# Performance work log

Hardware: AMD Instinct MI355X
Metric: run time of the kernel (lower is better)

The kernel has to match this reference:

```python
import jax, jax.numpy as jnp
import numpy as np

# Gemma config constants (layer_idx=0 -> 'sliding_attention')
H = 8          # num query heads
KVH = 4        # num kv heads
DH = 256       # head_dim
SW = 1024      # sliding_window
ROPE_BASE = 10000.0   # rope_local_base_freq (sliding layer)
EPS = 1e-6
SCALE = 256.0 ** -0.5  # query_pre_attn_scalar ** -0.5


def _rms_norm(x, w):
    # Gemma RMSNorm: fp32 norm, scale by (1 + w)
    x32 = x.astype(jnp.float32)
    n = x32 * jax.lax.rsqrt(jnp.mean(x32 * x32, axis=-1, keepdims=True) + EPS)
    return (n * (1.0 + w.astype(jnp.float32))).astype(x.dtype)


def _rope_cos_sin(S):
    inv_freq = 1.0 / (ROPE_BASE ** (jnp.arange(0, DH, 2, dtype=jnp.float32) / DH))
    freqs = jnp.outer(jnp.arange(S, dtype=jnp.float32), inv_freq)  # [S, DH/2]
    emb = jnp.concatenate([freqs, freqs], axis=-1)                 # [S, DH]
    return jnp.cos(emb), jnp.sin(emb)


def _rotate_half(x):
    x1, x2 = jnp.split(x, 2, axis=-1)
    return jnp.concatenate([-x2, x1], axis=-1)


def _apply_rope(x, cos, sin):
    # x: [B, H, S, DH]; cos/sin: [S, DH]
    return x * cos[None, None] + _rotate_half(x) * sin[None, None]


def setup_inputs() -> dict:
    key = jax.random.key(0)
    ks = jax.random.split(key, 7)
    B, S, D = 2, 2048, 2048
    w = lambda k, shape: jax.random.normal(k, shape, jnp.float32) * 0.02
    return {
        "hidden_states": jax.random.normal(ks[0], (B, S, D), jnp.float32),
        "Wq": w(ks[1], (H * DH, D)),
        "Wk": w(ks[2], (KVH * DH, D)),
        "Wv": w(ks[3], (KVH * DH, D)),
        "Wo": w(ks[4], (D, H * DH)),
        "q_norm_w": jnp.zeros((DH,), jnp.float32),
        "k_norm_w": jnp.zeros((DH,), jnp.float32),
    }


def reference(hidden_states, Wq, Wk, Wv, Wo, q_norm_w, k_norm_w):
    B, S, D = hidden_states.shape
    # projections (no bias)
    q = jnp.einsum("bsd,ed->bse", hidden_states, Wq).reshape(B, S, H, DH).transpose(0, 2, 1, 3)
    k = jnp.einsum("bsd,ed->bse", hidden_states, Wk).reshape(B, S, KVH, DH).transpose(0, 2, 1, 3)
    v = jnp.einsum("bsd,ed->bse", hidden_states, Wv).reshape(B, S, KVH, DH).transpose(0, 2, 1, 3)
    # Gemma q/k RMSNorm over head_dim, then RoPE (local base for sliding layer)
    q = _rms_norm(q, q_norm_w)
    k = _rms_norm(k, k_norm_w)
    cos, sin = _rope_cos_sin(S)
    q = _apply_rope(q, cos, sin)
    k = _apply_rope(k, cos, sin)
    # GQA: repeat kv heads
    rep = H // KVH
    k = jnp.repeat(k, rep, axis=1)
    v = jnp.repeat(v, rep, axis=1)
    # causal sliding-window mask
    i = jnp.arange(S)[:, None]
    j = jnp.arange(S)[None, :]
    mask = (j <= i) & (i - j < SW)  # [S, S]
    scores = jnp.einsum("bhqd,bhkd->bhqk", q, k) * SCALE
    scores = jnp.where(mask[None, None], scores, jnp.finfo(jnp.float32).min)
    attn = jax.nn.softmax(scores.astype(jnp.float32), axis=-1).astype(q.dtype)
    out = jnp.einsum("bhqk,bhkd->bhqd", attn, v)  # [B, H, S, DH]
    out = out.transpose(0, 2, 1, 3).reshape(B, S, H * DH)
    return jnp.einsum("bse,de->bsd", out, Wo)
```

## Files before the change

### kernel.cpp

```cpp
#include <hip/hip_runtime.h>
#include <hip/hip_bf16.h>


typedef __bf16 bf16x8 __attribute__((ext_vector_type(8)));
typedef __bf16 bf16x4 __attribute__((ext_vector_type(4)));
typedef float f32x4 __attribute__((ext_vector_type(4)));

#define NB 2
#define SEQ 2048
#define DMODEL 2048
#define NH 8
#define NKV 4
#define DHEAD 256
#define SWIN 1024

#define AS1 __attribute__((address_space(1)))
#define AS3 __attribute__((address_space(3)))

static __device__ __forceinline__ void gload_lds16(const void* g, void* l) {
    __builtin_amdgcn_global_load_lds((const AS1 void*)g, (AS3 void*)l, 16, 0, 0);
}

static __device__ __forceinline__ bf16x4 tr16(const __bf16* p) {
    bf16x4 r;
    asm volatile("ds_read_b64_tr_b16 %0, %1" : "=v"(r) : "v"((const AS3 __bf16*)p));
    return r;
}

__global__ void cvt_rope(const float* __restrict__ s0, const float* __restrict__ s1,
                         const float* __restrict__ s2, const float* __restrict__ s3,
                         const float* __restrict__ s4, __bf16* __restrict__ d0,
                         __bf16* __restrict__ d1, __bf16* __restrict__ d2,
                         __bf16* __restrict__ d3, __bf16* __restrict__ d4,
                         float* __restrict__ cosT, float* __restrict__ sinT) {
    if (blockIdx.x >= 20480) {
        int idx = (blockIdx.x - 20480) * 256 + threadIdx.x;
        int s = idx >> 7, i = idx & 127;
        float fr = (float)s * __expf(-(float)i * 0.0719557843f);
        cosT[idx] = cosf(fr);
        sinT[idx] = sinf(fr);
        return;
    }
    int i = blockIdx.x * 256 + threadIdx.x;
    const float* src; __bf16* dst;
    if (i < 2097152) { src = s0; dst = d0; }
    else if (i < 3145728) { i -= 2097152; src = s1; dst = d1; }
    else if (i < 3670016) { i -= 3145728; src = s2; dst = d2; }
    else if (i < 4194304) { i -= 3670016; src = s3; dst = d3; }
    else                  { i -= 4194304; src = s4; dst = d4; }
    f32x4 v = ((const f32x4*)src)[i];
    bf16x4 o;
#pragma unroll
    for (int j = 0; j < 4; ++j) o[j] = (__bf16)v[j];
    ((bf16x4*)dst)[i] = o;
}

template <int OUTBF16>
__global__ __launch_bounds__(512, 2)
void gemm_bt8(const __bf16* __restrict__ A, const __bf16* __restrict__ B,
              void* __restrict__ Cv, int M, int N, int K, int nbx) {
    __shared__ __align__(16) __bf16 sA[2][256 * 64];
    __shared__ __align__(16) __bf16 sB[2][256 * 64];
    const int tid = threadIdx.x;
    const int wave = tid >> 6, lane = tid & 63;
    const int lo = lane & 15, hi = lane >> 4;
    const int wm = wave >> 2, wn = wave & 3;
    const int qq = (int)gridDim.x >> 3;
    const int swz = ((int)blockIdx.x & 7) * qq + ((int)blockIdx.x >> 3);
    const int bx = swz % nbx, by = swz / nbx;
    const int brow = by * 256, bcol = bx * 256;
    const int xr = lo & 7;

    int aoff[4];
#pragma unroll
    for (int i = 0; i < 4; ++i) {
        int n = i * 512 + tid, r = n >> 3, s = n & 7;
        aoff[i] = r * K + ((s ^ (r & 7)) << 3);
    }
    const __bf16* Ab = A + (size_t)brow * K;
    const __bf16* Bb = B + (size_t)bcol * K;

    auto stgA = [&](int bsel, int kt, int h) {
        const __bf16* ga = Ab + kt * 64;
#pragma unroll
        for (int ii = 0; ii < 2; ++ii) {
            int i = h + ii * 2;
            gload_lds16(ga + aoff[i], (char*)&sA[bsel][0] + (i * 512 + wave * 64) * 16);
        }
    };
    auto stgB = [&](int bsel, int kt, int h) {
        const __bf16* gb = Bb + kt * 64;
#pragma unroll
        for (int i = 2 * h; i < 2 * h + 2; ++i)
            gload_lds16(gb + aoff[i], (char*)&sB[bsel][0] + (i * 512 + wave * 64) * 16);
    };

    f32x4 acc[8][4] = {};
    const int nt = K >> 6;

    stgA(0, 0, 0); stgA(0, 0, 1); stgB(0, 0, 0); stgB(0, 0, 1);
    stgA(1, 1, 0); stgA(1, 1, 1); stgB(1, 1, 0); stgB(1, 1, 1);
    asm volatile("s_waitcnt vmcnt(8)" ::: "memory");
    __builtin_amdgcn_s_barrier();

    for (int t = 0; t < nt; ++t) {
        const int buf = t & 1;
        const bool pre = (t + 2 < nt);
        const __bf16* sa = &sA[buf][0];
        const __bf16* sb = &sB[buf][0];
        bf16x8 af[8], b0[4], b1[4];
#pragma unroll
        for (int m = 0; m < 4; ++m)
#pragma unroll
            for (int ks = 0; ks < 2; ++ks)
                af[m * 2 + ks] = *(const bf16x8*)&sa[(wm * 128 + m * 16 + lo) * 64 + (((ks * 4 + hi) ^ xr) << 3)];
#pragma unroll
        for (int n = 0; n < 2; ++n)
#pragma unroll
            for (int ks = 0; ks < 2; ++ks)
                b0[n * 2 + ks] = *(const bf16x8*)&sb[(wn * 64 + n * 16 + lo) * 64 + (((ks * 4 + hi) ^ xr) << 3)];
        __builtin_amdgcn_sched_barrier(0);
        __builtin_amdgcn_s_barrier();
        __builtin_amdgcn_s_setprio(1);
#pragma unroll
        for (int m = 0; m < 4; ++m)
#pragma unroll
            for (int n = 0; n < 2; ++n)
#pragma unroll
                for (int ks = 0; ks < 2; ++ks)
                    acc[m][n] = __builtin_amdgcn_mfma_f32_16x16x32_bf16(af[m * 2 + ks], b0[n * 2 + ks], acc[m][n], 0, 0, 0);
        __builtin_amdgcn_s_setprio(0);
        __builtin_amdgcn_sched_barrier(0);
        __builtin_amdgcn_s_barrier();
#pragma unroll
        for (int n = 0; n < 2; ++n)
#pragma unroll
            for (int ks = 0; ks < 2; ++ks)
                b1[n * 2 + ks] = *(const bf16x8*)&sb[(wn * 64 + (n + 2) * 16 + lo) * 64 + (((ks * 4 + hi) ^ xr) << 3)];
        if (pre) stgA(buf, t + 2, 0);
        __builtin_amdgcn_sched_barrier(0);
        __builtin_amdgcn_s_barrier();
        __builtin_amdgcn_s_setprio(1);
#pragma unroll
        for (int m = 0; m < 4; ++m)
#pragma unroll
            for (int n = 0; n < 2; ++n)
#pragma unroll
                for (int ks = 0; ks < 2; ++ks)
                    acc[m][n + 2] = __builtin_amdgcn_mfma_f32_16x16x32_bf16(af[m * 2 + ks], b1[n * 2 + ks], acc[m][n + 2], 0, 0, 0);
        __builtin_amdgcn_s_setprio(0);
        __builtin_amdgcn_sched_barrier(0);
        __builtin_amdgcn_s_barrier();
#pragma unroll
        for (int m = 0; m < 4; ++m)
#pragma unroll
            for (int ks = 0; ks < 2; ++ks)
                af[m * 2 + ks] = *(const bf16x8*)&sa[(wm * 128 + (m + 4) * 16 + lo) * 64 + (((ks * 4 + hi) ^ xr) << 3)];
        if (pre) stgB(buf, t + 2, 1);
        __builtin_amdgcn_sched_barrier(0);
        __builtin_amdgcn_s_barrier();
        __builtin_amdgcn_s_setprio(1);
#pragma unroll
        for (int m = 0; m < 4; ++m)
#pragma unroll
            for (int n = 0; n < 2; ++n)
#pragma unroll
                for (int ks = 0; ks < 2; ++ks)
                    acc[m + 4][n + 2] = __builtin_amdgcn_mfma_f32_16x16x32_bf16(af[m * 2 + ks], b1[n * 2 + ks], acc[m + 4][n + 2], 0, 0, 0);
        __builtin_amdgcn_s_setprio(0);
        __builtin_amdgcn_sched_barrier(0);
        __builtin_amdgcn_s_barrier();
        if (pre) { stgA(buf, t + 2, 1); stgB(buf, t + 2, 0); }
        __builtin_amdgcn_sched_barrier(0);
        __builtin_amdgcn_s_setprio(1);
#pragma unroll
        for (int m = 0; m < 4; ++m)
#pragma unroll
            for (int n = 0; n < 2; ++n)
#pragma unroll
                for (int ks = 0; ks < 2; ++ks)
                    acc[m + 4][n] = __builtin_amdgcn_mfma_f32_16x16x32_bf16(af[m * 2 + ks], b0[n * 2 + ks], acc[m + 4][n], 0, 0, 0);
        __builtin_amdgcn_s_setprio(0);
        if (pre) asm volatile("s_waitcnt vmcnt(8)" ::: "memory");
        else     asm volatile("s_waitcnt vmcnt(0)" ::: "memory");
        __builtin_amdgcn_sched_barrier(0);
        __builtin_amdgcn_s_barrier();
    }

#pragma unroll
    for (int m = 0; m < 8; ++m) {
        int row = brow + wm * 128 + m * 16 + hi * 4;
#pragma unroll
        for (int n = 0; n < 4; ++n) {
            int col = bcol + wn * 64 + n * 16 + lo;
            if constexpr (OUTBF16) {
                __bf16* cp = (__bf16*)Cv + (size_t)row * N + col;
#pragma unroll
                for (int j = 0; j < 4; ++j)
                    cp[(size_t)j * N] = (__bf16)acc[m][n][j];
            } else {
                float* cp = (float*)Cv + (size_t)row * N + col;
#pragma unroll
                for (int j = 0; j < 4; ++j)
                    cp[(size_t)j * N] = acc[m][n][j];
            }
        }
    }
}

__global__ __launch_bounds__(512, 2)
void gemm_bt8n(const __bf16* __restrict__ A, const __bf16* __restrict__ B,
               float* __restrict__ C, int M, int N, int K, int nbx) {
    __shared__ __align__(16) __bf16 sA[2][256 * 64];
    __shared__ __align__(16) __bf16 sB[2][128 * 64];
    const int tid = threadIdx.x;
    const int wave = tid >> 6, lane = tid & 63;
    const int lo = lane & 15, hi = lane >> 4;
    const int wm = wave >> 1, wn = wave & 1;
    const int qq = (int)gridDim.x >> 3;
    const int swz = ((int)blockIdx.x & 7) * qq + ((int)blockIdx.x >> 3);
    const int bx = swz % nbx, by = swz / nbx;
    const int brow = by * 256, bcol = bx * 128;
    const int xr = lo & 7;

    int aoff[4], boff[2];
#pragma unroll
    for (int i = 0; i < 4; ++i) {
        int n = i * 512 + tid, r = n >> 3, s = n & 7;
        aoff[i] = r * K + ((s ^ (r & 7)) << 3);
    }
#pragma unroll
    for (int i = 0; i < 2; ++i) {
        int n = i * 512 + tid, r = n >> 3, s = n & 7;
        boff[i] = r * K + ((s ^ (r & 7)) << 3);
    }
    const __bf16* Ab = A + (size_t)brow * K;
    const __bf16* Bb = B + (size_t)bcol * K;

    auto stgAall = [&](int bsel, int kt) {
        const __bf16* ga = Ab + kt * 64;
#pragma unroll
        for (int i = 0; i < 4; ++i)
            gload_lds16(ga + aoff[i], (char*)&sA[bsel][0] + (i * 512 + wave * 64) * 16);
    };
    auto stgBall = [&](int bsel, int kt) {
        const __bf16* gb = Bb + kt * 64;
#pragma unroll
        for (int i = 0; i < 2; ++i)
            gload_lds16(gb + boff[i], (char*)&sB[bsel][0] + (i * 512 + wave * 64) * 16);
    };

    f32x4 acc[4][4] = {};
    const int nt = K >> 6;

    stgAall(0, 0); stgBall(0, 0);
    stgAall(1, 1); stgBall(1, 1);
    asm volatile("s_waitcnt vmcnt(6)" ::: "memory");
    __builtin_amdgcn_s_barrier();

    for (int t = 0; t < nt; ++t) {
        const int buf = t & 1;
        const bool pre = (t + 2 < nt);
        const __bf16* sa = &sA[buf][0];
        const __bf16* sb = &sB[buf][0];
        bf16x8 af[4], b0[4], b1[4];
#pragma unroll
        for (int m = 0; m < 2; ++m)
#pragma unroll
            for (int ks = 0; ks < 2; ++ks)
                af[m * 2 + ks] = *(const bf16x8*)&sa[(wm * 64 + m * 16 + lo) * 64 + (((ks * 4 + hi) ^ xr) << 3)];
#pragma unroll
        for (int n = 0; n < 2; ++n)
#pragma unroll
            for (int ks = 0; ks < 2; ++ks)
                b0[n * 2 + ks] = *(const bf16x8*)&sb[(wn * 64 + n * 16 + lo) * 64 + (((ks * 4 + hi) ^ xr) << 3)];
        __builtin_amdgcn_sched_barrier(0);
        __builtin_amdgcn_s_barrier();
        __builtin_amdgcn_s_setprio(1);
#pragma unroll
        for (int m = 0; m < 2; ++m)
#pragma unroll
            for (int n = 0; n < 2; ++n)
#pragma unroll
                for (int ks = 0; ks < 2; ++ks)
                    acc[m][n] = __builtin_amdgcn_mfma_f32_16x16x32_bf16(af[m * 2 + ks], b0[n * 2 + ks], acc[m][n], 0, 0, 0);
        __builtin_amdgcn_s_setprio(0);
        __builtin_amdgcn_sched_barrier(0);
        __builtin_amdgcn_s_barrier();
#pragma unroll
        for (int n = 0; n < 2; ++n)
#pragma unroll
            for (int ks = 0; ks < 2; ++ks)
                b1[n * 2 + ks] = *(const bf16x8*)&sb[(wn * 64 + (n + 2) * 16 + lo) * 64 + (((ks * 4 + hi) ^ xr) << 3)];
        __builtin_amdgcn_sched_barrier(0);
        __builtin_amdgcn_s_barrier();
        __builtin_amdgcn_s_setprio(1);
#pragma unroll
        for (int m = 0; m < 2; ++m)
#pragma unroll
            for (int n = 0; n < 2; ++n)
#pragma unroll
                for (int ks = 0; ks < 2; ++ks)
                    acc[m][n + 2] = __builtin_amdgcn_mfma_f32_16x16x32_bf16(af[m * 2 + ks], b1[n * 2 + ks], acc[m][n + 2], 0, 0, 0);
        __builtin_amdgcn_s_setprio(0);
        __builtin_amdgcn_sched_barrier(0);
        __builtin_amdgcn_s_barrier();
#pragma unroll
        for (int m = 0; m < 2; ++m)
#pragma unroll
            for (int ks = 0; ks < 2; ++ks)
                af[m * 2 + ks] = *(const bf16x8*)&sa[(wm * 64 + (m + 2) * 16 + lo) * 64 + (((ks * 4 + hi) ^ xr) << 3)];
        if (pre) stgBall(buf, t + 2);
        __builtin_amdgcn_sched_barrier(0);
        __builtin_amdgcn_s_barrier();
        __builtin_amdgcn_s_setprio(1);
#pragma unroll
        for (int m = 0; m < 2; ++m)
#pragma unroll
            for (int n = 0; n < 2; ++n)
#pragma unroll
                for (int ks = 0; ks < 2; ++ks)
                    acc[m + 2][n + 2] = __builtin_amdgcn_mfma_f32_16x16x32_bf16(af[m * 2 + ks], b1[n * 2 + ks], acc[m + 2][n + 2], 0, 0, 0);
        __builtin_amdgcn_s_setprio(0);
        __builtin_amdgcn_sched_barrier(0);
        __builtin_amdgcn_s_barrier();
        if (pre) stgAall(buf, t + 2);
        __builtin_amdgcn_sched_barrier(0);
        __builtin_amdgcn_s_setprio(1);
#pragma unroll
        for (int m = 0; m < 2; ++m)
#pragma unroll
            for (int n = 0; n < 2; ++n)
#pragma unroll
                for (int ks = 0; ks < 2; ++ks)
                    acc[m + 2][n] = __builtin_amdgcn_mfma_f32_16x16x32_bf16(af[m * 2 + ks], b0[n * 2 + ks], acc[m + 2][n], 0, 0, 0);
        __builtin_amdgcn_s_setprio(0);
        if (pre) asm volatile("s_waitcnt vmcnt(6)" ::: "memory");
        else     asm volatile("s_waitcnt vmcnt(0)" ::: "memory");
        __builtin_amdgcn_sched_barrier(0);
        __builtin_amdgcn_s_barrier();
    }

#pragma unroll
    for (int m = 0; m < 4; ++m) {
        int row = brow + wm * 64 + m * 16 + hi * 4;
#pragma unroll
        for (int n = 0; n < 4; ++n) {
            float* cp = C + (size_t)row * N + bcol + wn * 64 + n * 16 + lo;
#pragma unroll
            for (int j = 0; j < 4; ++j)
                cp[(size_t)j * N] = acc[m][n][j];
        }
    }
}

__global__ __launch_bounds__(256)
void norm_rope(const __bf16* __restrict__ QKV, const float* __restrict__ qw,
               const float* __restrict__ kw, const float* __restrict__ cosT,
               const float* __restrict__ sinT, __bf16* __restrict__ Qo,
               __bf16* __restrict__ Ko, __bf16* __restrict__ Vo) {
    const int r = blockIdx.x;
    const int b = r >> 11, s = r & (SEQ - 1);
    const int wave = threadIdx.x >> 6, lane = threadIdx.x & 63;
    f32x4 cos4 = *(const f32x4*)&cosT[s * 128 + (lane & 31) * 4];
    f32x4 sin4 = *(const f32x4*)&sinT[s * 128 + (lane & 31) * 4];
#pragma unroll
    for (int ii = 0; ii < 4; ++ii) {
        int hh = wave + ii * 4;
        if (hh < 12) {
            bool isq = hh < 8;
            int col0 = isq ? hh * DHEAD : DMODEL + (hh - 8) * DHEAD;
            const __bf16* src = QKV + (size_t)r * 4096 + col0;
            bf16x4 xb = *(const bf16x4*)&src[lane * 4];
            float x[4];
#pragma unroll
            for (int j = 0; j < 4; ++j) x[j] = (float)xb[j];
            float ss = x[0] * x[0] + x[1] * x[1] + x[2] * x[2] + x[3] * x[3];
#pragma unroll
            for (int d2 = 1; d2 < 64; d2 <<= 1) ss += __shfl_xor(ss, d2);
            float scale = rsqrtf(ss * (1.f / DHEAD) + 1e-6f);
            const float* wp = isq ? qw : kw;
            float nx[4];
#pragma unroll
            for (int j = 0; j < 4; ++j)
                nx[j] = x[j] * scale * (1.f + wp[lane * 4 + j]);
            bf16x4 ov;
#pragma unroll
            for (int j = 0; j < 4; ++j) {
                float other = __shfl_xor(nx[j], 32);
                float rot = (lane < 32) ? -other : other;
                float v = nx[j] * cos4[j] + rot * sin4[j];
                if (isq) v *= 0.0625f;
                ov[j] = (__bf16)v;
            }
            __bf16* dst = isq ? (Qo + ((size_t)(b * NH + hh) * SEQ + s) * DHEAD)
                              : (Ko + ((size_t)(b * NKV + (hh - 8)) * SEQ + s) * DHEAD);
            *(bf16x4*)&dst[lane * 4] = ov;
        } else {
            int vh = hh - 12;
            const __bf16* src = QKV + (size_t)r * 4096 + 3072 + vh * DHEAD;
            bf16x4 xb = *(const bf16x4*)&src[lane * 4];
            __bf16* dst = Vo + ((size_t)(b * NKV + vh) * SEQ + s) * DHEAD;
            *(bf16x4*)&dst[lane * 4] = xb;
        }
    }
}

__global__ __launch_bounds__(256)
void attn7(const __bf16* __restrict__ Q, const __bf16* __restrict__ Kb,
           const __bf16* __restrict__ Vb, __bf16* __restrict__ ctx) {
    const int bid = blockIdx.x;
    const int bk = bid & 7;
    const int qt = 63 - (bid >> 3);
    const int b = bk >> 2, kh = bk & 3;
    const int q0 = qt * 32;
    const int tid = threadIdx.x;
    const int wave = tid >> 6, lane = tid & 63;
    const int lo = lane & 15, hi = lane >> 4;
    const int hsel = wave >> 1, qsub = wave & 1;
    const int h = kh * 2 + hsel;
    const int qbase = q0 + qsub * 16;
    const int q = qbase + lo;

    __shared__ __align__(16) __bf16 kbuf[2][32 * 256];
    __shared__ __align__(16) __bf16 vbuf[2][32 * 256];

    const __bf16* Qp = Q + ((size_t)(b * NH + h) * SEQ + qbase) * DHEAD;
    const __bf16* Kp = Kb + (size_t)(b * NKV + kh) * SEQ * DHEAD;
    const __bf16* Vp = Vb + (size_t)(b * NKV + kh) * SEQ * DHEAD;

    int koff[4], voff[4];
#pragma unroll
    for (int i = 0; i < 4; ++i) {
        int n = i * 256 + tid;
        int r = n >> 5, c = n & 31;
        koff[i] = r * 256 + ((c ^ (r & 7)) << 3);
        int st = n >> 3, w = n & 7;
        int vk = (st & 7) * 4 + (w >> 1);
        int vd = (st >> 3) * 16 + (w & 1) * 8;
        voff[i] = vk * 256 + vd;
    }

    auto stage = [&](int bsel, int c0) {
        const __bf16* kg = Kp + (size_t)c0 * DHEAD;
        const __bf16* vg = Vp + (size_t)c0 * DHEAD;
        char* kd = (char*)&kbuf[bsel][0] + wave * 1024;
        char* vd = (char*)&vbuf[bsel][0] + wave * 1024;
#pragma unroll
        for (int i = 0; i < 4; ++i) {
            gload_lds16(kg + koff[i], kd + i * 4096);
            gload_lds16(vg + voff[i], vd + i * 4096);
        }
    };

    bf16x8 qf[8];
#pragma unroll
    for (int dc = 0; dc < 8; ++dc)
        qf[dc] = *(const bf16x8*)(Qp + (size_t)lo * DHEAD + dc * 32 + hi * 8);

    f32x4 o[16] = {};
    float m = -3e38f, l = 0.f;

    int kstart = q0 - SWIN; if (kstart < 0) kstart = 0;
    const int nt = (q0 + 32 - kstart) >> 5;

    stage(0, kstart);
    asm volatile("s_waitcnt vmcnt(0)" ::: "memory");
    __builtin_amdgcn_sched_barrier(0);
    __builtin_amdgcn_s_barrier();
    __builtin_amdgcn_sched_barrier(0);

    for (int t = 0; t < nt; ++t) {
        const int c0 = kstart + t * 32;
        const int buf = t & 1;
        const bool pre = (t + 1 < nt);
        if (pre) stage(buf ^ 1, c0 + 32);

        f32x4 sc0 = {}, sc1 = {};
        const __bf16* kb0 = &kbuf[buf][0];
        __builtin_amdgcn_s_setprio(1);
#pragma unroll
        for (int dc = 0; dc < 8; ++dc) {
            int u = dc * 4 + hi;
            bf16x8 kfa = *(const bf16x8*)&kb0[lo * 256 + ((u ^ (lo & 7)) << 3)];
            bf16x8 kfb = *(const bf16x8*)&kb0[(16 + lo) * 256 + ((u ^ ((16 + lo) & 7)) << 3)];
            sc0 = __builtin_amdgcn_mfma_f32_16x16x32_bf16(kfa, qf[dc], sc0, 0, 0, 0);
            sc1 = __builtin_amdgcn_mfma_f32_16x16x32_bf16(kfb, qf[dc], sc1, 0, 0, 0);
        }
        __builtin_amdgcn_s_setprio(0);

        float s8[8];
#pragma unroll
        for (int j = 0; j < 4; ++j) {
            int ka = c0 + hi * 4 + j;
            int kb2 = ka + 16;
            s8[j]     = (ka <= q && q - ka < SWIN) ? sc0[j] : -1e30f;
            s8[4 + j] = (kb2 <= q && q - kb2 < SWIN) ? sc1[j] : -1e30f;
        }
        float pm = s8[0];
#pragma unroll
        for (int i = 1; i < 8; ++i) pm = fmaxf(pm, s8[i]);
        pm = fmaxf(pm, __shfl_xor(pm, 16));
        pm = fmaxf(pm, __shfl_xor(pm, 32));
        if (__any(pm > m + 8.f)) {
            float mn = fmaxf(m, pm);
            float corr = __expf(m - mn);
            l *= corr;
#pragma unroll
            for (int dt = 0; dt < 16; ++dt) o[dt] *= corr;
            m = mn;
        }
        float p8[8], ps = 0.f;
#pragma unroll
        for (int i = 0; i < 8; ++i) {
            float e = __expf(s8[i] - m);
            p8[i] = (s8[i] > -9e29f) ? e : 0.f;
            ps += p8[i];
        }
        ps += __shfl_xor(ps, 16);
        ps += __shfl_xor(ps, 32);
        l += ps;

        bf16x8 paf;
#pragma unroll
        for (int i = 0; i < 8; ++i) paf[i] = (__bf16)p8[i];

        const __bf16* vb0 = &vbuf[buf][0];
#pragma unroll
        for (int dq = 0; dq < 4; ++dq) {
            bf16x4 t0[4], t1[4];
#pragma unroll
            for (int u = 0; u < 4; ++u) {
                int dt = dq * 4 + u;
                t0[u] = tr16(vb0 + (dt * 8 + hi) * 64 + lo * 4);
                t1[u] = tr16(vb0 + (dt * 8 + 4 + hi) * 64 + lo * 4);
            }
            asm volatile("s_waitcnt lgkmcnt(0)" ::: "memory");
            __builtin_amdgcn_sched_barrier(0);
            __builtin_amdgcn_s_setprio(1);
#pragma unroll
            for (int u = 0; u < 4; ++u) {
                bf16x8 vf;
#pragma unroll
                for (int j = 0; j < 4; ++j) { vf[j] = t0[u][j]; vf[4 + j] = t1[u][j]; }
                o[dq * 4 + u] = __builtin_amdgcn_mfma_f32_16x16x32_bf16(vf, paf, o[dq * 4 + u], 0, 0, 0);
            }
            __builtin_amdgcn_s_setprio(0);
        }

        if (pre) {
            asm volatile("s_waitcnt vmcnt(0)" ::: "memory");
            __builtin_amdgcn_sched_barrier(0);
            __builtin_amdgcn_s_barrier();
            __builtin_amdgcn_sched_barrier(0);
        }
    }

    const float invl = 1.0f / l;
    __bf16* cp = ctx + ((size_t)(b * SEQ + q)) * (NH * DHEAD) + h * DHEAD;
#pragma unroll
    for (int dt = 0; dt < 16; ++dt) {
        bf16x4 w;
#pragma unroll
        for (int j = 0; j < 4; ++j) w[j] = (__bf16)(o[dt][j] * invl);
        *(bf16x4*)&cp[dt * 16 + hi * 4] = w;
    }
}

extern "C" void kernel_launch(void* const* d_in, const int* in_sizes, int n_in,
                              void* d_out, int out_size, void* d_ws, size_t ws_size,
                              hipStream_t stream) {
    const float* hs = (const float*)d_in[0];
    const float* Wq = (const float*)d_in[1];
    const float* Wk = (const float*)d_in[2];
    const float* Wv = (const float*)d_in[3];
    const float* Wo = (const float*)d_in[4];
    const float* qw = (const float*)d_in[5];
    const float* kw = (const float*)d_in[6];
    float* out = (float*)d_out;

    char* ws = (char*)d_ws;
    size_t off = 0;
    auto alloc = [&](size_t bytes) {
        char* p = ws + off;
        off += (bytes + 255) & ~(size_t)255;
        return p;
    };
    const int M = NB * SEQ;
    __bf16* hsB   = (__bf16*)alloc((size_t)M * DMODEL * 2);
    __bf16* WqkvB = (__bf16*)alloc((size_t)4096 * DMODEL * 2);
    __bf16* WoB   = (__bf16*)alloc((size_t)DMODEL * DMODEL * 2);
    __bf16* QKVb  = (__bf16*)alloc((size_t)M * 4096 * 2);
    __bf16* Qb    = (__bf16*)alloc((size_t)M * 2048 * 2);
    __bf16* Kbf   = (__bf16*)alloc((size_t)M * 1024 * 2);
    __bf16* Vbf   = (__bf16*)alloc((size_t)M * 1024 * 2);
    float*  cosT  = (float*) alloc((size_t)SEQ * 128 * 4);
    float*  sinT  = (float*) alloc((size_t)SEQ * 128 * 4);
    __bf16* ctxB  = QKVb;

    cvt_rope<<<21504, 256, 0, stream>>>(hs, Wq, Wk, Wv, Wo,
                                        hsB, WqkvB, WqkvB + (size_t)2048 * 2048,
                                        WqkvB + (size_t)3072 * 2048, WoB, cosT, sinT);

    gemm_bt8<1><<<256, 512, 0, stream>>>(hsB, WqkvB, QKVb, M, 4096, DMODEL, 16);

    norm_rope<<<M, 256, 0, stream>>>(QKVb, qw, kw, cosT, sinT, Qb, Kbf, Vbf);

    attn7<<<512, 256, 0, stream>>>(Qb, Kbf, Vbf, ctxB);

    gemm_bt8n<<<256, 512, 0, stream>>>(ctxB, WoB, out, M, DMODEL, DMODEL, 16);
}
```

Before: 213.2 us.

## Split key tiles across two wave groups per attention block and merge

Attention blocks now use 512 threads, with two halves each processing half of the sliding-window key tiles using separate LDS buffers. Partial softmax states (m, l, o) are merged through LDS at the end. This halves the serial per-block tile loop and doubles the waves available. In exchange it drops the prefetch double-buffering in favour of stage-then-sync each iteration, and adds the merge cost.

```diff
diff --git a/kernel.cpp b/kernel.cpp
--- a/kernel.cpp
+++ b/kernel.cpp
@@ -406,8 +406,8 @@
     }
 }
 
-__global__ __launch_bounds__(256)
-void attn7(const __bf16* __restrict__ Q, const __bf16* __restrict__ Kb,
+__global__ __launch_bounds__(512, 4)
+void attn9(const __bf16* __restrict__ Q, const __bf16* __restrict__ Kb,
            const __bf16* __restrict__ Vb, __bf16* __restrict__ ctx) {
     const int bid = blockIdx.x;
     const int bk = bid & 7;
@@ -417,13 +417,16 @@
     const int tid = threadIdx.x;
     const int wave = tid >> 6, lane = tid & 63;
     const int lo = lane & 15, hi = lane >> 4;
-    const int hsel = wave >> 1, qsub = wave & 1;
+    const int half = wave >> 2, hq = wave & 3;
+    const int hsel = hq >> 1, qsub = hq & 1;
     const int h = kh * 2 + hsel;
     const int qbase = q0 + qsub * 16;
     const int q = qbase + lo;
-
-    __shared__ __align__(16) __bf16 kbuf[2][32 * 256];
-    __shared__ __align__(16) __bf16 vbuf[2][32 * 256];
+    const int lt = tid & 255;
+    const int lw = hq;
+
+    __shared__ __align__(16) __bf16 kv[4][32 * 256];
+    __shared__ float mlb[4][2][16];
 
     const __bf16* Qp = Q + ((size_t)(b * NH + h) * SEQ + qbase) * DHEAD;
     const __bf16* Kp = Kb + (size_t)(b * NKV + kh) * SEQ * DHEAD;
@@ -432,7 +435,7 @@
     int koff[4], voff[4];
 #pragma unroll
     for (int i = 0; i < 4; ++i) {
-        int n = i * 256 + tid;
+        int n = i * 256 + lt;
         int r = n >> 5, c = n & 31;
         koff[i] = r * 256 + ((c ^ (r & 7)) << 3);
         int st = n >> 3, w = n & 7;
@@ -441,11 +444,11 @@
         voff[i] = vk * 256 + vd;
     }
 
-    auto stage = [&](int bsel, int c0) {
+    auto stage = [&](int c0) {
         const __bf16* kg = Kp + (size_t)c0 * DHEAD;
         const __bf16* vg = Vp + (size_t)c0 * DHEAD;
-        char* kd = (char*)&kbuf[bsel][0] + wave * 1024;
-        char* vd = (char*)&vbuf[bsel][0] + wave * 1024;
+        char* kd = (char*)&kv[2 * half][0] + lw * 1024;
+        char* vd = (char*)&kv[2 * half + 1][0] + lw * 1024;
 #pragma unroll
         for (int i = 0; i < 4; ++i) {
             gload_lds16(kg + koff[i], kd + i * 4096);
@@ -463,107 +466,115 @@
 
     int kstart = q0 - SWIN; if (kstart < 0) kstart = 0;
     const int nt = (q0 + 32 - kstart) >> 5;
-
-    stage(0, kstart);
-    asm volatile("s_waitcnt vmcnt(0)" ::: "memory");
-    __builtin_amdgcn_sched_barrier(0);
-    __builtin_amdgcn_s_barrier();
-    __builtin_amdgcn_sched_barrier(0);
-
-    for (int t = 0; t < nt; ++t) {
-        const int c0 = kstart + t * 32;
-        const int buf = t & 1;
-        const bool pre = (t + 1 < nt);
-        if (pre) stage(buf ^ 1, c0 + 32);
-
-        f32x4 sc0 = {}, sc1 = {};
-        const __bf16* kb0 = &kbuf[buf][0];
-        __builtin_amdgcn_s_setprio(1);
-#pragma unroll
-        for (int dc = 0; dc < 8; ++dc) {
-            int u = dc * 4 + hi;
-            bf16x8 kfa = *(const bf16x8*)&kb0[lo * 256 + ((u ^ (lo & 7)) << 3)];
-            bf16x8 kfb = *(const bf16x8*)&kb0[(16 + lo) * 256 + ((u ^ ((16 + lo) & 7)) << 3)];
-            sc0 = __builtin_amdgcn_mfma_f32_16x16x32_bf16(kfa, qf[dc], sc0, 0, 0, 0);
-            sc1 = __builtin_amdgcn_mfma_f32_16x16x32_bf16(kfb, qf[dc], sc1, 0, 0, 0);
-        }
-        __builtin_amdgcn_s_setprio(0);
-
-        float s8[8];
-#pragma unroll
-        for (int j = 0; j < 4; ++j) {
-            int ka = c0 + hi * 4 + j;
-            int kb2 = ka + 16;
-            s8[j]     = (ka <= q && q - ka < SWIN) ? sc0[j] : -1e30f;
-            s8[4 + j] = (kb2 <= q && q - kb2 < SWIN) ? sc1[j] : -1e30f;
-        }
-        float pm = s8[0];
-#pragma unroll
-        for (int i = 1; i < 8; ++i) pm = fmaxf(pm, s8[i]);
-        pm = fmaxf(pm, __shfl_xor(pm, 16));
-        pm = fmaxf(pm, __shfl_xor(pm, 32));
-        if (__any(pm > m + 8.f)) {
-            float mn = fmaxf(m, pm);
-            float corr = __expf(m - mn);
-            l *= corr;
-#pragma unroll
-            for (int dt = 0; dt < 16; ++dt) o[dt] *= corr;
-            m = mn;
-        }
-        float p8[8], ps = 0.f;
-#pragma unroll
-        for (int i = 0; i < 8; ++i) {
-            float e = __expf(s8[i] - m);
-            p8[i] = (s8[i] > -9e29f) ? e : 0.f;
-            ps += p8[i];
-        }
-        ps += __shfl_xor(ps, 16);
-        ps += __shfl_xor(ps, 32);
-        l += ps;
-
-        bf16x8 paf;
-#pragma unroll
-        for (int i = 0; i < 8; ++i) paf[i] = (__bf16)p8[i];
-
-        const __bf16* vb0 = &vbuf[buf][0];
-#pragma unroll
-        for (int dq = 0; dq < 4; ++dq) {
-            bf16x4 t0[4], t1[4];
-#pragma unroll
-            for (int u = 0; u < 4; ++u) {
-                int dt = dq * 4 + u;
-                t0[u] = tr16(vb0 + (dt * 8 + hi) * 64 + lo * 4);
-                t1[u] = tr16(vb0 + (dt * 8 + 4 + hi) * 64 + lo * 4);
-            }
-            asm volatile("s_waitcnt lgkmcnt(0)" ::: "memory");
-            __builtin_amdgcn_sched_barrier(0);
+    const int nh = (nt + 1) >> 1;
+
+    for (int i = 0; i < nh; ++i) {
+        const int tt = half ? (nh + i) : i;
+        const bool valid = half ? (tt < nt) : true;
+        const int c0 = kstart + tt * 32;
+        if (valid) stage(c0);
+        __syncthreads();
+
+        if (valid) {
+            f32x4 sc0 = {}, sc1 = {};
+            const __bf16* kb0 = &kv[2 * half][0];
             __builtin_amdgcn_s_setprio(1);
 #pragma unroll
-            for (int u = 0; u < 4; ++u) {
-                bf16x8 vf;
-#pragma unroll
-                for (int j = 0; j < 4; ++j) { vf[j] = t0[u][j]; vf[4 + j] = t1[u][j]; }
-                o[dq * 4 + u] = __builtin_amdgcn_mfma_f32_16x16x32_bf16(vf, paf, o[dq * 4 + u], 0, 0, 0);
+            for (int dc = 0; dc < 8; ++dc) {
+                int u = dc * 4 + hi;
+                bf16x8 kfa = *(const bf16x8*)&kb0[lo * 256 + ((u ^ (lo & 7)) << 3)];
+                bf16x8 kfb = *(const bf16x8*)&kb0[(16 + lo) * 256 + ((u ^ ((16 + lo) & 7)) << 3)];
+                sc0 = __builtin_amdgcn_mfma_f32_16x16x32_bf16(kfa, qf[dc], sc0, 0, 0, 0);
+                sc1 = __builtin_amdgcn_mfma_f32_16x16x32_bf16(kfb, qf[dc], sc1, 0, 0, 0);
             }
             __builtin_amdgcn_s_setprio(0);
+
+            float s8[8];
+#pragma unroll
+            for (int j = 0; j < 4; ++j) {
+                int ka = c0 + hi * 4 + j;
+                int kb2 = ka + 16;
+                s8[j]     = (ka <= q && q - ka < SWIN) ? sc0[j] : -1e30f;
+                s8[4 + j] = (kb2 <= q && q - kb2 < SWIN) ? sc1[j] : -1e30f;
+            }
+            float pm = s8[0];
+#pragma unroll
+            for (int i2 = 1; i2 < 8; ++i2) pm = fmaxf(pm, s8[i2]);
+            pm = fmaxf(pm, __shfl_xor(pm, 16));
+            pm = fmaxf(pm, __shfl_xor(pm, 32));
+            if (__any(pm > m + 8.f)) {
+                float mn = fmaxf(m, pm);
+                float corr = __expf(m - mn);
+                l *= corr;
+#pragma unroll
+                for (int dt = 0; dt < 16; ++dt) o[dt] *= corr;
+                m = mn;
+            }
+            float p8[8], ps = 0.f;
+#pragma unroll
+            for (int i2 = 0; i2 < 8; ++i2) {
+                float e = __expf(s8[i2] - m);
+                p8[i2] = (s8[i2] > -9e29f) ? e : 0.f;
+                ps += p8[i2];
+            }
+            ps += __shfl_xor(ps, 16);
+            ps += __shfl_xor(ps, 32);
+            l += ps;
+
+            bf16x8 paf;
+#pragma unroll
+            for (int i2 = 0; i2 < 8; ++i2) paf[i2] = (__bf16)p8[i2];
+
+            const __bf16* vb0 = &kv[2 * half + 1][0];
+#pragma unroll
+            for (int dq = 0; dq < 4; ++dq) {
+                bf16x4 t0[4], t1[4];
+#pragma unroll
+                for (int u = 0; u < 4; ++u) {
+                    int dt = dq * 4 + u;
+                    t0[u] = tr16(vb0 + (dt * 8 + hi) * 64 + lo * 4);
+                    t1[u] = tr16(vb0 + (dt * 8 + 4 + hi) * 64 + lo * 4);
+                }
+                asm volatile("s_waitcnt lgkmcnt(0)" ::: "memory");
+                __builtin_amdgcn_sched_barrier(0);
+                __builtin_amdgcn_s_setprio(1);
+#pragma unroll
+                for (int u = 0; u < 4; ++u) {
+                    bf16x8 vf;
+#pragma unroll
+                    for (int j = 0; j < 4; ++j) { vf[j] = t0[u][j]; vf[4 + j] = t1[u][j]; }
+                    o[dq * 4 + u] = __builtin_amdgcn_mfma_f32_16x16x32_bf16(vf, paf, o[dq * 4 + u], 0, 0, 0);
+                }
+                __builtin_amdgcn_s_setprio(0);
+            }
         }
-
-        if (pre) {
-            asm volatile("s_waitcnt vmcnt(0)" ::: "memory");
-            __builtin_amdgcn_sched_barrier(0);
-            __builtin_amdgcn_s_barrier();
-            __builtin_amdgcn_sched_barrier(0);
+        __syncthreads();
+    }
+
+    float* mbase = (float*)&kv[0][0] + hq * 4096;
+    if (half == 1) {
+#pragma unroll
+        for (int dt = 0; dt < 16; ++dt)
+            *(f32x4*)&mbase[lo * 256 + dt * 16 + hi * 4] = o[dt];
+        if (hi == 0) { mlb[hq][0][lo] = m; mlb[hq][1][lo] = l; }
+    }
+    __syncthreads();
+    if (half == 0) {
+        float m1 = mlb[hq][0][lo], l1 = mlb[hq][1][lo];
+        float ms = fmaxf(m, m1);
+        float c0f = __expf(m - ms), c1f = __expf(m1 - ms);
+        float lt2 = l * c0f + l1 * c1f;
+        float invl = 1.0f / lt2;
+        __bf16* cp = ctx + ((size_t)(b * SEQ + q)) * (NH * DHEAD) + h * DHEAD;
+#pragma unroll
+        for (int dt = 0; dt < 16; ++dt) {
+            f32x4 v1 = *(const f32x4*)&mbase[lo * 256 + dt * 16 + hi * 4];
+            bf16x4 w;
+#pragma unroll
+            for (int j = 0; j < 4; ++j)
+                w[j] = (__bf16)((o[dt][j] * c0f + v1[j] * c1f) * invl);
+            *(bf16x4*)&cp[dt * 16 + hi * 4] = w;
         }
-    }
-
-    const float invl = 1.0f / l;
-    __bf16* cp = ctx + ((size_t)(b * SEQ + q)) * (NH * DHEAD) + h * DHEAD;
-#pragma unroll
-    for (int dt = 0; dt < 16; ++dt) {
-        bf16x4 w;
-#pragma unroll
-        for (int j = 0; j < 4; ++j) w[j] = (__bf16)(o[dt][j] * invl);
-        *(bf16x4*)&cp[dt * 16 + hi * 4] = w;
     }
 }
 
@@ -606,7 +617,7 @@
 
     norm_rope<<<M, 256, 0, stream>>>(QKVb, qw, kw, cosT, sinT, Qb, Kbf, Vbf);
 
-    attn7<<<512, 256, 0, stream>>>(Qb, Kbf, Vbf, ctxB);
+    attn9<<<512, 512, 0, stream>>>(Qb, Kbf, Vbf, ctxB);
 
     gemm_bt8n<<<256, 512, 0, stream>>>(ctxB, WoB, out, M, DMODEL, DMODEL, 16);
 }
```

Result: slower. 410.7 us (+92.7%).
